# Optimization experiments

Hardware: AMD Instinct MI355X
Metric: run time of the kernel (lower is better)

Reference implementation:

```python
import jax, jax.numpy as jnp
import numpy as np

D_MODEL, D_LOW, NUM_BINS = 512, 64, 39
DIST_MIN, DIST_MAX = 2.0, 22.0
BIN_WIDTH = (DIST_MAX - DIST_MIN) / (NUM_BINS - 1)
LN_EPS = 1e-5


def setup_inputs() -> dict:
    key = jax.random.key(0)
    ks = jax.random.split(key, 10)
    B, N = 2, 768
    h_res = jax.random.normal(ks[0], (B, N, D_MODEL), dtype=jnp.float32)
    # scale coords so pairwise distances span the [2, 22] bin range
    x_true = jax.random.normal(ks[1], (B, N, 3), dtype=jnp.float32) * 5.0
    token_pad_mask = jnp.ones((B, N), dtype=jnp.float32)
    s = 1.0 / np.sqrt(D_MODEL)
    return {
        "h_res": h_res,
        "x_true": x_true,
        "token_pad_mask": token_pad_mask,
        "ln_w": jnp.ones((D_MODEL,), jnp.float32),
        "ln_b": jnp.zeros((D_MODEL,), jnp.float32),
        "wu_w": jax.random.normal(ks[2], (D_LOW, D_MODEL), jnp.float32) * s,
        "wu_b": jnp.zeros((D_LOW,), jnp.float32),
        "wv_w": jax.random.normal(ks[3], (D_LOW, D_MODEL), jnp.float32) * s,
        "wv_b": jnp.zeros((D_LOW,), jnp.float32),
        "wb_w": jax.random.normal(ks[4], (NUM_BINS, D_LOW), jnp.float32) * (1.0 / np.sqrt(D_LOW)),
        "wb_b": jnp.zeros((NUM_BINS,), jnp.float32),
    }


def _layernorm(x, w, b):
    mu = jnp.mean(x, axis=-1, keepdims=True)
    var = jnp.mean(jnp.square(x - mu), axis=-1, keepdims=True)
    return (x - mu) * jax.lax.rsqrt(var + LN_EPS) * w + b


def reference(h_res, x_true, token_pad_mask, ln_w, ln_b, wu_w, wu_b, wv_w, wv_b, wb_w, wb_b):
    B, N, _ = h_res.shape
    # pairwise distances -> target bins (trunc-to-int then clamp, as torch .long())
    diff = x_true[:, :, None, :] - x_true[:, None, :, :]          # [B,N,N,3]
    d_true = jnp.sqrt(jnp.sum(diff * diff, axis=-1))               # [B,N,N]
    target = jnp.clip(((d_true - DIST_MIN) / BIN_WIDTH).astype(jnp.int32), 0, NUM_BINS - 1)

    h = _layernorm(h_res, ln_w, ln_b)
    U = h @ wu_w.T + wu_b                                          # [B,N,d_low]
    V = h @ wv_w.T + wv_b                                          # [B,N,d_low]
    # logits[b,i,j,k] = sum_c U[b,i,c] V[b,j,c] Wb[k,c] + bb[k]
    logits = jnp.einsum("bic,bjc,kc->bijk", U, V, wb_w) + wb_b     # [B,N,N,K]
    logp = jax.nn.log_softmax(logits, axis=-1)
    ce = -jnp.take_along_axis(logp, target[..., None], axis=-1)[..., 0]  # [B,N,N]

    mask = (token_pad_mask[:, :, None] * token_pad_mask[:, None, :]) > 0  # [B,N,N] bool
    counts = jnp.sum(mask, axis=(1, 2))                            # [B]
    per_sample = jnp.sum(jnp.where(mask, ce, 0.0), axis=(1, 2)) / jnp.maximum(counts, 1)
    valid = counts > 0
    total_count = jnp.sum(valid)
    loss = jnp.sum(jnp.where(valid, per_sample, 0.0)) / jnp.maximum(total_count, 1)
    return loss
```

## Files before the change

kernel.cpp:

```cpp
#include <hip/hip_runtime.h>
#include <hip/hip_bf16.h>
#include <math.h>

#define D_MODEL 512
#define D_LOW   64
#define NBINS   39
#define LOG2E   1.4426950408889634f
#define LN2     0.6931471805599453f

typedef __attribute__((ext_vector_type(8))) short short8;
typedef __attribute__((ext_vector_type(4))) float floatx4;

__global__ __launch_bounds__(256) void prep_kernel(
    const float* __restrict__ ln_w, const float* __restrict__ ln_b,
    const float* __restrict__ wu_w, const float* __restrict__ wu_b,
    const float* __restrict__ wv_w, const float* __restrict__ wv_b,
    __hip_bfloat16* __restrict__ w2bf, float* __restrict__ w2sum,
    float* __restrict__ b2) {
  __shared__ float red[8];
  const int tid = threadIdx.x;
  const int o = blockIdx.x;
  const bool isU = (o < 64);
  const float* wrow = isU ? (wu_w + o * D_MODEL) : (wv_w + (o - 64) * D_MODEL);
  const float scale = isU ? LOG2E : 1.0f;

  float s1 = 0.f, s2 = 0.f;
  #pragma unroll
  for (int cc = 0; cc < 2; ++cc) {
    const int c = tid + cc * 256;
    const float w  = wrow[c];
    const float w2 = w * ln_w[c] * scale;
    const __hip_bfloat16 hb = __float2bfloat16(w2);
    w2bf[o * D_MODEL + c] = hb;
    s1 += __bfloat162float(hb);
    s2 += w * ln_b[c];
  }
  #pragma unroll
  for (int off = 32; off; off >>= 1) {
    s1 += __shfl_xor(s1, off);
    s2 += __shfl_xor(s2, off);
  }
  const int wave = tid >> 6, lane = tid & 63;
  if (lane == 0) { red[wave] = s1; red[4 + wave] = s2; }
  __syncthreads();
  if (tid == 0) {
    w2sum[o] = red[0] + red[1] + red[2] + red[3];
    const float ss2 = red[4] + red[5] + red[6] + red[7];
    b2[o] = scale * ((isU ? wu_b[o] : wv_b[o - 64]) + ss2);
  }
}

__global__ __launch_bounds__(256) void lnproj_wprep_kernel(
    const float* __restrict__ h_res, const __hip_bfloat16* __restrict__ w2bf,
    const float* __restrict__ w2sum, const float* __restrict__ b2,
    const float* __restrict__ wb_w,
    __hip_bfloat16* __restrict__ Vbf, short* __restrict__ wfragbuf, int N) {
  __shared__ float Urow[16][D_LOW];
  __shared__ float wsh[NBINS * 65];
  const int tid  = threadIdx.x;
  const int wave = tid >> 6, lane = tid & 63;
  const int q = lane >> 4, ln16 = lane & 15;
  const int row0 = blockIdx.x * 16;

  for (int e = tid; e < NBINS * D_LOW; e += 256) {
    wsh[(e >> 6) * 65 + (e & 63)] = wb_w[e];
  }

  const float* hp = h_res + (size_t)(row0 + ln16) * D_MODEL + q * 8;
  short8 abf[16];
  float sum = 0.f, ssq = 0.f;
  #pragma unroll
  for (int kc = 0; kc < 16; ++kc) {
    const floatx4 x0 = *reinterpret_cast<const floatx4*>(hp + kc * 32);
    const floatx4 x1 = *reinterpret_cast<const floatx4*>(hp + kc * 32 + 4);
    short8 a;
    #pragma unroll
    for (int e = 0; e < 4; ++e) {
      sum += x0[e]; ssq += x0[e] * x0[e];
      const __hip_bfloat16 hb = __float2bfloat16(x0[e]);
      a[e] = *reinterpret_cast<const short*>(&hb);
    }
    #pragma unroll
    for (int e = 0; e < 4; ++e) {
      sum += x1[e]; ssq += x1[e] * x1[e];
      const __hip_bfloat16 hb = __float2bfloat16(x1[e]);
      a[4 + e] = *reinterpret_cast<const short*>(&hb);
    }
    abf[kc] = a;
  }
  sum += __shfl_xor(sum, 16); sum += __shfl_xor(sum, 32);
  ssq += __shfl_xor(ssq, 16); ssq += __shfl_xor(ssq, 32);
  const float mu  = sum * (1.0f / (float)D_MODEL);
  const float var = ssq * (1.0f / (float)D_MODEL) - mu * mu;
  const float rs  = rsqrtf(var + 1e-5f);
  float mu_r[4], rs_r[4];
  #pragma unroll
  for (int r = 0; r < 4; ++r) {
    mu_r[r] = __shfl(mu, q * 4 + r);
    rs_r[r] = __shfl(rs, q * 4 + r);
  }

  const int obase = wave * 32;
  const int out0 = obase + ln16;
  const int out1 = obase + 16 + ln16;
  const short* wp = reinterpret_cast<const short*>(w2bf);
  floatx4 acc0 = (floatx4){0.f, 0.f, 0.f, 0.f};
  floatx4 acc1 = (floatx4){0.f, 0.f, 0.f, 0.f};
  #pragma unroll
  for (int kc = 0; kc < 16; ++kc) {
    const short8 b0 = *reinterpret_cast<const short8*>(
        wp + (size_t)out0 * D_MODEL + kc * 32 + q * 8);
    const short8 b1 = *reinterpret_cast<const short8*>(
        wp + (size_t)out1 * D_MODEL + kc * 32 + q * 8);
    acc0 = __builtin_amdgcn_mfma_f32_16x16x32_bf16(abf[kc], b0, acc0, 0, 0, 0);
    acc1 = __builtin_amdgcn_mfma_f32_16x16x32_bf16(abf[kc], b1, acc1, 0, 0, 0);
  }

  #pragma unroll
  for (int nt = 0; nt < 2; ++nt) {
    const int out  = nt ? out1 : out0;
    const floatx4 a = nt ? acc1 : acc0;
    const float ws = w2sum[out];
    const float bb = b2[out];
    #pragma unroll
    for (int r = 0; r < 4; ++r) {
      const int rloc = q * 4 + r;
      const float val = rs_r[r] * a[r] - mu_r[r] * rs_r[r] * ws + bb;
      if (out < 64) {
        Urow[rloc][out] = val;
      } else {
        Vbf[(size_t)(row0 + rloc) * D_LOW + (out - 64)] = __float2bfloat16(val);
      }
    }
  }
  __syncthreads();

  #pragma unroll
  for (int rr = 0; rr < 4; ++rr) {
    const int rloc = wave * 4 + rr;
    const int rowi = row0 + rloc;
    float u[16];
    #pragma unroll
    for (int s = 0; s < 2; ++s)
      #pragma unroll
      for (int e = 0; e < 8; ++e) u[s * 8 + e] = Urow[rloc][s * 32 + q * 8 + e];
    short* outp = wfragbuf + (size_t)rowi * 6 * 64 * 8;
    #pragma unroll
    for (int t = 0; t < 3; ++t) {
      const int n = t * 16 + ln16;
      #pragma unroll
      for (int s = 0; s < 2; ++s) {
        short8 f;
        #pragma unroll
        for (int e = 0; e < 8; ++e) {
          const float w = (n < NBINS) ? wsh[n * 65 + s * 32 + q * 8 + e] : 0.f;
          const float v = u[s * 8 + e] * w;
          const __hip_bfloat16 hb = __float2bfloat16(v);
          f[e] = *reinterpret_cast<const short*>(&hb);
        }
        *reinterpret_cast<short8*>(outp + ((size_t)(t * 2 + s) * 64 + lane) * 8) = f;
      }
    }
  }
}

__global__ __launch_bounds__(256) void pair_mfma_kernel(
    const short* __restrict__ wfragbuf,
    const __hip_bfloat16* __restrict__ Vbf,
    const float* __restrict__ x_true, const float* __restrict__ pmask,
    const float* __restrict__ wb_b,
    float* __restrict__ part, int N) {
  __shared__ int tbm[768];
  __shared__ float rbuf[8];
  const int i = blockIdx.x, b = blockIdx.y;
  const int tid  = threadIdx.x;
  const int wave = tid >> 6, lane = tid & 63;
  const int q = lane >> 4, ln16 = lane & 15;
  const int rowi = b * N + i;

  {
    const float xi0 = x_true[rowi * 3 + 0];
    const float xi1 = x_true[rowi * 3 + 1];
    const float xi2 = x_true[rowi * 3 + 2];
    const float pmi = pmask[rowi];
    const float BW  = (22.0f - 2.0f) / 38.0f;
    for (int j = tid; j < N; j += 256) {
      const int rowj = b * N + j;
      const float dx = xi0 - x_true[rowj * 3 + 0];
      const float dy = xi1 - x_true[rowj * 3 + 1];
      const float dz = xi2 - x_true[rowj * 3 + 2];
      const float d  = sqrtf(dx * dx + dy * dy + dz * dz);
      int tb = (int)((d - 2.0f) / BW);
      tb = tb < 0 ? 0 : (tb > NBINS - 1 ? NBINS - 1 : tb);
      tbm[j] = (pmi * pmask[rowj] > 0.f) ? tb : -1;
    }
  }

  short8 wfrag[3][2];
  {
    const short* wfp = wfragbuf + (size_t)rowi * 6 * 64 * 8;
    #pragma unroll
    for (int t = 0; t < 3; ++t)
      #pragma unroll
      for (int s = 0; s < 2; ++s)
        wfrag[t][s] = *reinterpret_cast<const short8*>(
            wfp + ((size_t)(t * 2 + s) * 64 + lane) * 8);
  }

  floatx4 bias_init[3];
  #pragma unroll
  for (int t = 0; t < 3; ++t)
    #pragma unroll
    for (int r = 0; r < 4; ++r) {
      const int bin = t * 16 + q * 4 + r;
      bias_init[t][r] = (bin < NBINS) ? LOG2E * wb_b[bin] : -INFINITY;
    }

  __syncthreads();

  const short* Vp = reinterpret_cast<const short*>(Vbf) + (size_t)b * N * D_LOW;
  const int jbase = wave * 192;
  const int q4 = q * 4;

  float ce_sum = 0.f, cnt_sum = 0.f;

  short8 v[2][2];
  int tbv[2];
  #pragma unroll
  for (int tt = 0; tt < 2; ++tt) {
    const size_t jr = jbase + tt * 16 + ln16;
    v[tt][0] = *reinterpret_cast<const short8*>(Vp + jr * D_LOW + q * 8);
    v[tt][1] = *reinterpret_cast<const short8*>(Vp + jr * D_LOW + 32 + q * 8);
    tbv[tt]  = tbm[jr];
  }

  for (int g = 0; g < 6; ++g) {
    short8 vn[2][2];
    int tbn[2];
    if (g < 5) {
      const int jb = jbase + (g + 1) * 32;
      #pragma unroll
      for (int tt = 0; tt < 2; ++tt) {
        const size_t jr = jb + tt * 16 + ln16;
        vn[tt][0] = *reinterpret_cast<const short8*>(Vp + jr * D_LOW + q * 8);
        vn[tt][1] = *reinterpret_cast<const short8*>(Vp + jr * D_LOW + 32 + q * 8);
        tbn[tt]   = tbm[jr];
      }
    }

    floatx4 f[2][3];
    #pragma unroll
    for (int tt = 0; tt < 2; ++tt)
      #pragma unroll
      for (int t = 0; t < 3; ++t) {
        floatx4 a = bias_init[t];
        a = __builtin_amdgcn_mfma_f32_16x16x32_bf16(wfrag[t][0], v[tt][0], a, 0, 0, 0);
        a = __builtin_amdgcn_mfma_f32_16x16x32_bf16(wfrag[t][1], v[tt][1], a, 0, 0, 0);
        f[tt][t] = a;
      }

    #pragma unroll
    for (int tt = 0; tt < 2; ++tt) {
      const int tb  = tbv[tt];
      const int tbq = tb - q4;
      float s0 = 0.f, s1 = 0.f, s2 = 0.f, s3 = 0.f, lt = 0.f;
      #pragma unroll
      for (int t = 0; t < 3; ++t) {
        const floatx4 fv = f[tt][t];
        s0 += __builtin_amdgcn_exp2f(fv[0]);
        s1 += __builtin_amdgcn_exp2f(fv[1]);
        s2 += __builtin_amdgcn_exp2f(fv[2]);
        s3 += __builtin_amdgcn_exp2f(fv[3]);
        lt += (tbq == t * 16 + 0) ? fv[0] : 0.f;
        lt += (tbq == t * 16 + 1) ? fv[1] : 0.f;
        lt += (tbq == t * 16 + 2) ? fv[2] : 0.f;
        lt += (tbq == t * 16 + 3) ? fv[3] : 0.f;
      }
      float ssum = (s0 + s1) + (s2 + s3);
      ssum += __shfl_xor(ssum, 16); ssum += __shfl_xor(ssum, 32);
      const float ok = (tb >= 0) ? 1.f : 0.f;
      ce_sum  += ok * LN2 * (__builtin_amdgcn_logf(ssum) - 4.0f * lt);
      cnt_sum += ok;
    }

    if (g < 5) {
      #pragma unroll
      for (int tt = 0; tt < 2; ++tt) {
        v[tt][0] = vn[tt][0]; v[tt][1] = vn[tt][1]; tbv[tt] = tbn[tt];
      }
    }
  }

  #pragma unroll
  for (int off = 32; off; off >>= 1) {
    ce_sum  += __shfl_xor(ce_sum, off);
    cnt_sum += __shfl_xor(cnt_sum, off);
  }
  if (lane == 0) { rbuf[wave] = ce_sum; rbuf[4 + wave] = cnt_sum; }
  __syncthreads();
  if (tid == 0) {
    part[rowi * 2 + 0] = rbuf[0] + rbuf[1] + rbuf[2] + rbuf[3];
    part[rowi * 2 + 1] = rbuf[4] + rbuf[5] + rbuf[6] + rbuf[7];
  }
}

__global__ __launch_bounds__(256) void finalize_kernel(
    const float* __restrict__ part, float* __restrict__ out, int N, int B) {
  __shared__ float red[8];
  const int tid = threadIdx.x, wave = tid >> 6, lane = tid & 63;
  float loss = 0.f, vcount = 0.f;
  for (int b = 0; b < B; ++b) {
    float ce = 0.f, cnt = 0.f;
    for (int i = tid; i < N; i += 256) {
      ce  += part[(b * N + i) * 2 + 0];
      cnt += part[(b * N + i) * 2 + 1];
    }
    #pragma unroll
    for (int off = 32; off; off >>= 1) {
      ce  += __shfl_xor(ce, off);
      cnt += __shfl_xor(cnt, off);
    }
    if (lane == 0) { red[wave] = ce; red[4 + wave] = cnt; }
    __syncthreads();
    if (tid == 0) {
      const float s = red[0] + red[1] + red[2] + red[3];
      const float c = red[4] + red[5] + red[6] + red[7];
      if (c > 0.f) { loss += s / fmaxf(c, 1.f); vcount += 1.f; }
    }
    __syncthreads();
  }
  if (tid == 0) out[0] = (vcount > 0.f) ? loss / vcount : 0.f;
}

extern "C" void kernel_launch(void* const* d_in, const int* in_sizes, int n_in,
                              void* d_out, int out_size, void* d_ws, size_t ws_size,
                              hipStream_t stream) {
  const float* h_res  = (const float*)d_in[0];
  const float* x_true = (const float*)d_in[1];
  const float* pmask  = (const float*)d_in[2];
  const float* ln_w   = (const float*)d_in[3];
  const float* ln_b   = (const float*)d_in[4];
  const float* wu_w   = (const float*)d_in[5];
  const float* wu_b   = (const float*)d_in[6];
  const float* wv_w   = (const float*)d_in[7];
  const float* wv_b   = (const float*)d_in[8];
  const float* wb_w   = (const float*)d_in[9];
  const float* wb_b   = (const float*)d_in[10];

  const int B  = 2;
  const int N  = in_sizes[2] / B;
  const int BN = B * N;

  __hip_bfloat16* Vbf = (__hip_bfloat16*)d_ws;
  float* part = (float*)(Vbf + (size_t)BN * D_LOW);
  short* wfragbuf = (short*)(part + 2 * (size_t)BN);
  __hip_bfloat16* w2bf = (__hip_bfloat16*)(wfragbuf + (size_t)BN * 6 * 64 * 8);
  float* w2sum = (float*)(w2bf + 128 * D_MODEL);
  float* b2    = w2sum + 128;

  prep_kernel<<<128, 256, 0, stream>>>(ln_w, ln_b, wu_w, wu_b, wv_w, wv_b,
                                       w2bf, w2sum, b2);
  lnproj_wprep_kernel<<<BN / 16, 256, 0, stream>>>(h_res, w2bf, w2sum, b2,
                                                   wb_w, Vbf, wfragbuf, N);
  pair_mfma_kernel<<<dim3(N, B), 256, 0, stream>>>(wfragbuf, Vbf, x_true,
                                                   pmask, wb_b, part, N);
  finalize_kernel<<<1, 256, 0, stream>>>(part, (float*)d_out, N, B);
}
```

Baseline: 123.2 us.

## Precompute distance bins in prep kernel and tile pair kernel over two rows

Target-bin computation moves out of the pair kernel into extra blocks of the prep kernel, which write an int8 [B,N,N] bin map to global memory. The pair kernel now processes two i rows per block, reusing each loaded V fragment for both rows. It splits j across two blocks and writes per-wave partial sums, so the LDS table and the block-level syncs disappear. This adds global traffic for the bin map and more partials for finalize to reduce. The explicit V prefetch double-buffering is also dropped, which may expose load latency.

```diff
diff --git a/kernel.cpp b/kernel.cpp
--- a/kernel.cpp
+++ b/kernel.cpp
@@ -11,14 +11,40 @@
 typedef __attribute__((ext_vector_type(8))) short short8;
 typedef __attribute__((ext_vector_type(4))) float floatx4;
 
-__global__ __launch_bounds__(256) void prep_kernel(
+__global__ __launch_bounds__(256) void prep_tbin_kernel(
     const float* __restrict__ ln_w, const float* __restrict__ ln_b,
     const float* __restrict__ wu_w, const float* __restrict__ wu_b,
     const float* __restrict__ wv_w, const float* __restrict__ wv_b,
+    const float* __restrict__ x_true, const float* __restrict__ pmask,
     __hip_bfloat16* __restrict__ w2bf, float* __restrict__ w2sum,
-    float* __restrict__ b2) {
+    float* __restrict__ b2, signed char* __restrict__ tbg, int N) {
+  const int tid = threadIdx.x;
+
+  if ((int)blockIdx.x >= 128) {
+    const int p = blockIdx.x - 128;
+    const int b = (p >= N) ? 1 : 0;
+    const int i = p - b * N;
+    const int rowi = b * N + i;
+    const float xi0 = x_true[rowi * 3 + 0];
+    const float xi1 = x_true[rowi * 3 + 1];
+    const float xi2 = x_true[rowi * 3 + 2];
+    const float pmi = pmask[rowi];
+    const float BW  = (22.0f - 2.0f) / 38.0f;
+    signed char* tbp = tbg + (size_t)b * N * N + (size_t)i * N;
+    for (int j = tid; j < N; j += 256) {
+      const int rowj = b * N + j;
+      const float dx = xi0 - x_true[rowj * 3 + 0];
+      const float dy = xi1 - x_true[rowj * 3 + 1];
+      const float dz = xi2 - x_true[rowj * 3 + 2];
+      const float d  = sqrtf(dx * dx + dy * dy + dz * dz);
+      int tb = (int)((d - 2.0f) / BW);
+      tb = tb < 0 ? 0 : (tb > NBINS - 1 ? NBINS - 1 : tb);
+      tbp[j] = (pmi * pmask[rowj] > 0.f) ? (signed char)tb : (signed char)-1;
+    }
+    return;
+  }
+
   __shared__ float red[8];
-  const int tid = threadIdx.x;
   const int o = blockIdx.x;
   const bool isU = (o < 64);
   const float* wrow = isU ? (wu_w + o * D_MODEL) : (wv_w + (o - 64) * D_MODEL);
@@ -167,43 +193,26 @@
 __global__ __launch_bounds__(256) void pair_mfma_kernel(
     const short* __restrict__ wfragbuf,
     const __hip_bfloat16* __restrict__ Vbf,
-    const float* __restrict__ x_true, const float* __restrict__ pmask,
     const float* __restrict__ wb_b,
+    const signed char* __restrict__ tbg,
     float* __restrict__ part, int N) {
-  __shared__ int tbm[768];
-  __shared__ float rbuf[8];
-  const int i = blockIdx.x, b = blockIdx.y;
+  const int p    = blockIdx.x;
+  const int b    = blockIdx.y >> 1;
+  const int half = blockIdx.y & 1;
   const int tid  = threadIdx.x;
   const int wave = tid >> 6, lane = tid & 63;
   const int q = lane >> 4, ln16 = lane & 15;
-  const int rowi = b * N + i;
-
-  {
-    const float xi0 = x_true[rowi * 3 + 0];
-    const float xi1 = x_true[rowi * 3 + 1];
-    const float xi2 = x_true[rowi * 3 + 2];
-    const float pmi = pmask[rowi];
-    const float BW  = (22.0f - 2.0f) / 38.0f;
-    for (int j = tid; j < N; j += 256) {
-      const int rowj = b * N + j;
-      const float dx = xi0 - x_true[rowj * 3 + 0];
-      const float dy = xi1 - x_true[rowj * 3 + 1];
-      const float dz = xi2 - x_true[rowj * 3 + 2];
-      const float d  = sqrtf(dx * dx + dy * dy + dz * dz);
-      int tb = (int)((d - 2.0f) / BW);
-      tb = tb < 0 ? 0 : (tb > NBINS - 1 ? NBINS - 1 : tb);
-      tbm[j] = (pmi * pmask[rowj] > 0.f) ? tb : -1;
-    }
-  }
-
-  short8 wfrag[3][2];
-  {
-    const short* wfp = wfragbuf + (size_t)rowi * 6 * 64 * 8;
+  const int row0 = b * N + p * 2;
+
+  short8 wfrag[2][3][2];
+  #pragma unroll
+  for (int ii = 0; ii < 2; ++ii) {
+    const short* wfp = wfragbuf + (size_t)(row0 + ii) * 6 * 64 * 8;
     #pragma unroll
     for (int t = 0; t < 3; ++t)
       #pragma unroll
       for (int s = 0; s < 2; ++s)
-        wfrag[t][s] = *reinterpret_cast<const short8*>(
+        wfrag[ii][t][s] = *reinterpret_cast<const short8*>(
             wfp + ((size_t)(t * 2 + s) * 64 + lane) * 8);
   }
 
@@ -216,91 +225,77 @@
       bias_init[t][r] = (bin < NBINS) ? LOG2E * wb_b[bin] : -INFINITY;
     }
 
-  __syncthreads();
-
   const short* Vp = reinterpret_cast<const short*>(Vbf) + (size_t)b * N * D_LOW;
-  const int jbase = wave * 192;
+  const signed char* tbp0 = tbg + (size_t)b * N * N + (size_t)(p * 2) * N;
+  const signed char* tbp1 = tbp0 + N;
+  const int jbase = half * 384 + wave * 96;
   const int q4 = q * 4;
 
-  float ce_sum = 0.f, cnt_sum = 0.f;
-
-  short8 v[2][2];
-  int tbv[2];
-  #pragma unroll
-  for (int tt = 0; tt < 2; ++tt) {
-    const size_t jr = jbase + tt * 16 + ln16;
-    v[tt][0] = *reinterpret_cast<const short8*>(Vp + jr * D_LOW + q * 8);
-    v[tt][1] = *reinterpret_cast<const short8*>(Vp + jr * D_LOW + 32 + q * 8);
-    tbv[tt]  = tbm[jr];
-  }
-
-  for (int g = 0; g < 6; ++g) {
-    short8 vn[2][2];
-    int tbn[2];
-    if (g < 5) {
-      const int jb = jbase + (g + 1) * 32;
+  float ce_acc[2] = {0.f, 0.f}, cnt_acc[2] = {0.f, 0.f};
+
+  for (int g = 0; g < 3; ++g) {
+    const int jb = jbase + g * 32;
+    short8 v[2][2];
+    int tbv[2][2];
+    #pragma unroll
+    for (int tt = 0; tt < 2; ++tt) {
+      const size_t jr = jb + tt * 16 + ln16;
+      v[tt][0] = *reinterpret_cast<const short8*>(Vp + jr * D_LOW + q * 8);
+      v[tt][1] = *reinterpret_cast<const short8*>(Vp + jr * D_LOW + 32 + q * 8);
+      tbv[0][tt] = (int)tbp0[jr];
+      tbv[1][tt] = (int)tbp1[jr];
+    }
+
+    #pragma unroll
+    for (int ii = 0; ii < 2; ++ii) {
       #pragma unroll
       for (int tt = 0; tt < 2; ++tt) {
-        const size_t jr = jb + tt * 16 + ln16;
-        vn[tt][0] = *reinterpret_cast<const short8*>(Vp + jr * D_LOW + q * 8);
-        vn[tt][1] = *reinterpret_cast<const short8*>(Vp + jr * D_LOW + 32 + q * 8);
-        tbn[tt]   = tbm[jr];
+        floatx4 f[3];
+        #pragma unroll
+        for (int t = 0; t < 3; ++t) {
+          floatx4 a = bias_init[t];
+          a = __builtin_amdgcn_mfma_f32_16x16x32_bf16(wfrag[ii][t][0], v[tt][0], a, 0, 0, 0);
+          a = __builtin_amdgcn_mfma_f32_16x16x32_bf16(wfrag[ii][t][1], v[tt][1], a, 0, 0, 0);
+          f[t] = a;
+        }
+        const int tb  = tbv[ii][tt];
+        const int tbq = tb - q4;
+        float s0 = 0.f, s1 = 0.f, s2 = 0.f, s3 = 0.f, lt = 0.f;
+        #pragma unroll
+        for (int t = 0; t < 3; ++t) {
+          const floatx4 fv = f[t];
+          s0 += __builtin_amdgcn_exp2f(fv[0]);
+          s1 += __builtin_amdgcn_exp2f(fv[1]);
+          s2 += __builtin_amdgcn_exp2f(fv[2]);
+          s3 += __builtin_amdgcn_exp2f(fv[3]);
+          lt += (tbq == t * 16 + 0) ? fv[0] : 0.f;
+          lt += (tbq == t * 16 + 1) ? fv[1] : 0.f;
+          lt += (tbq == t * 16 + 2) ? fv[2] : 0.f;
+          lt += (tbq == t * 16 + 3) ? fv[3] : 0.f;
+        }
+        float ssum = (s0 + s1) + (s2 + s3);
+        ssum += __shfl_xor(ssum, 16); ssum += __shfl_xor(ssum, 32);
+        const float ok = (tb >= 0) ? 1.f : 0.f;
+        ce_acc[ii]  += ok * LN2 * (__builtin_amdgcn_logf(ssum) - 4.0f * lt);
+        cnt_acc[ii] += ok;
       }
     }
-
-    floatx4 f[2][3];
-    #pragma unroll
-    for (int tt = 0; tt < 2; ++tt)
-      #pragma unroll
-      for (int t = 0; t < 3; ++t) {
-        floatx4 a = bias_init[t];
-        a = __builtin_amdgcn_mfma_f32_16x16x32_bf16(wfrag[t][0], v[tt][0], a, 0, 0, 0);
-        a = __builtin_amdgcn_mfma_f32_16x16x32_bf16(wfrag[t][1], v[tt][1], a, 0, 0, 0);
-        f[tt][t] = a;
-      }
-
-    #pragma unroll
-    for (int tt = 0; tt < 2; ++tt) {
-      const int tb  = tbv[tt];
-      const int tbq = tb - q4;
-      float s0 = 0.f, s1 = 0.f, s2 = 0.f, s3 = 0.f, lt = 0.f;
-      #pragma unroll
-      for (int t = 0; t < 3; ++t) {
-        const floatx4 fv = f[tt][t];
-        s0 += __builtin_amdgcn_exp2f(fv[0]);
-        s1 += __builtin_amdgcn_exp2f(fv[1]);
-        s2 += __builtin_amdgcn_exp2f(fv[2]);
-        s3 += __builtin_amdgcn_exp2f(fv[3]);
-        lt += (tbq == t * 16 + 0) ? fv[0] : 0.f;
-        lt += (tbq == t * 16 + 1) ? fv[1] : 0.f;
-        lt += (tbq == t * 16 + 2) ? fv[2] : 0.f;
-        lt += (tbq == t * 16 + 3) ? fv[3] : 0.f;
-      }
-      float ssum = (s0 + s1) + (s2 + s3);
-      ssum += __shfl_xor(ssum, 16); ssum += __shfl_xor(ssum, 32);
-      const float ok = (tb >= 0) ? 1.f : 0.f;
-      ce_sum  += ok * LN2 * (__builtin_amdgcn_logf(ssum) - 4.0f * lt);
-      cnt_sum += ok;
-    }
-
-    if (g < 5) {
-      #pragma unroll
-      for (int tt = 0; tt < 2; ++tt) {
-        v[tt][0] = vn[tt][0]; v[tt][1] = vn[tt][1]; tbv[tt] = tbn[tt];
-      }
-    }
   }
 
   #pragma unroll
   for (int off = 32; off; off >>= 1) {
-    ce_sum  += __shfl_xor(ce_sum, off);
-    cnt_sum += __shfl_xor(cnt_sum, off);
-  }
-  if (lane == 0) { rbuf[wave] = ce_sum; rbuf[4 + wave] = cnt_sum; }
-  __syncthreads();
-  if (tid == 0) {
-    part[rowi * 2 + 0] = rbuf[0] + rbuf[1] + rbuf[2] + rbuf[3];
-    part[rowi * 2 + 1] = rbuf[4] + rbuf[5] + rbuf[6] + rbuf[7];
+    ce_acc[0]  += __shfl_xor(ce_acc[0], off);
+    ce_acc[1]  += __shfl_xor(ce_acc[1], off);
+    cnt_acc[0] += __shfl_xor(cnt_acc[0], off);
+    cnt_acc[1] += __shfl_xor(cnt_acc[1], off);
+  }
+  if (lane == 0) {
+    #pragma unroll
+    for (int ii = 0; ii < 2; ++ii) {
+      const size_t slot = (((size_t)(row0 + ii) * 2 + half) * 4 + wave) * 2;
+      part[slot + 0] = ce_acc[ii];
+      part[slot + 1] = cnt_acc[ii];
+    }
   }
 }
 
@@ -311,9 +306,10 @@
   float loss = 0.f, vcount = 0.f;
   for (int b = 0; b < B; ++b) {
     float ce = 0.f, cnt = 0.f;
-    for (int i = tid; i < N; i += 256) {
-      ce  += part[(b * N + i) * 2 + 0];
-      cnt += part[(b * N + i) * 2 + 1];
+    for (int e = tid; e < 8 * N; e += 256) {
+      const size_t base = (size_t)b * 16 * N + (size_t)e * 2;
+      ce  += part[base + 0];
+      cnt += part[base + 1];
     }
     #pragma unroll
     for (int off = 32; off; off >>= 1) {
@@ -353,16 +349,18 @@
 
   __hip_bfloat16* Vbf = (__hip_bfloat16*)d_ws;
   float* part = (float*)(Vbf + (size_t)BN * D_LOW);
-  short* wfragbuf = (short*)(part + 2 * (size_t)BN);
+  signed char* tbg = (signed char*)(part + 16 * (size_t)BN);
+  short* wfragbuf = (short*)(tbg + (size_t)B * N * N);
   __hip_bfloat16* w2bf = (__hip_bfloat16*)(wfragbuf + (size_t)BN * 6 * 64 * 8);
   float* w2sum = (float*)(w2bf + 128 * D_MODEL);
   float* b2    = w2sum + 128;
 
-  prep_kernel<<<128, 256, 0, stream>>>(ln_w, ln_b, wu_w, wu_b, wv_w, wv_b,
-                                       w2bf, w2sum, b2);
+  prep_tbin_kernel<<<128 + BN, 256, 0, stream>>>(
+      ln_w, ln_b, wu_w, wu_b, wv_w, wv_b, x_true, pmask,
+      w2bf, w2sum, b2, tbg, N);
   lnproj_wprep_kernel<<<BN / 16, 256, 0, stream>>>(h_res, w2bf, w2sum, b2,
                                                    wb_w, Vbf, wfragbuf, N);
-  pair_mfma_kernel<<<dim3(N, B), 256, 0, stream>>>(wfragbuf, Vbf, x_true,
-                                                   pmask, wb_b, part, N);
+  pair_mfma_kernel<<<dim3(N / 2, 2 * B), 256, 0, stream>>>(wfragbuf, Vbf,
+                                                           wb_b, tbg, part, N);
   finalize_kernel<<<1, 256, 0, stream>>>(part, (float*)d_out, N, B);
 }
```

Measured after the change: 126.5 us. 1.03x slower.
